# Optimization experiments

Measured on AMD Instinct MI355X. Metric: run time of the kernel, lower is better.

## Reference

```python
import jax, jax.numpy as jnp
import numpy as np

EPS = 1e-5  # torch BatchNorm1d default eps
NH, KD, D_V = 8, 64, 128  # num_heads, key_dim, per-head value dim (attn_ratio*key_dim)


def hardswish(x):
    return x * jnp.clip(x + 3.0, 0.0, 6.0) / 6.0


def linear_bn(x, W, g, b):
    # Linear (no bias) followed by BatchNorm1d in training mode: batch stats
    # over all leading dims (torch flattens (B,N) before BN).
    y = x @ W.T
    yf = y.reshape(-1, y.shape[-1])
    mu = yf.mean(0)
    var = yf.var(0)  # biased variance, matching BN normalization
    return (y - mu) * (g / jnp.sqrt(var + EPS)) + b


def setup_inputs() -> dict:
    key = jax.random.key(0)
    ks = jax.random.split(key, 22)
    B, C, H, W, NT, D = 8, 1024, 96, 96, 60, 512
    dh = NH * D_V          # 1024
    h_kv = dh + NH * KD    # 1536
    hf = 2 * D             # 1024 (mr=2)

    def p(k, shape, s=0.02):
        return jax.random.normal(k, shape, jnp.float32) * s

    return {
        "im_emd": jax.random.normal(ks[0], (B, C, H, W), jnp.float32),
        "text_emd": jax.random.normal(ks[1], (NT, D), jnp.float32),
        "W_dc": p(ks[2], (D, C)), "g_dc": 1.0 + p(ks[3], (D,)), "b_dc": p(ks[4], (D,)),
        "W_kv": p(ks[5], (h_kv, D)), "g_kv": 1.0 + p(ks[6], (h_kv,)), "b_kv": p(ks[7], (h_kv,)),
        "W_q": p(ks[8], (NH * KD, D)), "g_q": 1.0 + p(ks[9], (NH * KD,)), "b_q": p(ks[10], (NH * KD,)),
        "W_proj": p(ks[11], (D, dh)), "g_proj": 1.0 + p(ks[12], (D,)), "b_proj": p(ks[13], (D,)),
        "biases": p(ks[14], (NH, 10000)),  # relative-position bias table (100x100 offsets)
        "W_f1": p(ks[15], (hf, D)), "g_f1": 1.0 + p(ks[16], (hf,)), "b_f1": p(ks[17], (hf,)),
        "W_f2": p(ks[18], (D, hf)), "g_f2": 1.0 + p(ks[19], (D,)), "b_f2": p(ks[20], (D,)),
    }


def _bias_idx(NT, H, W):
    # Offset table built row-major over product(range(100), range(100)) =>
    # attention_offsets[(a,b)] == 100*a + b. Text token t maps to grid point
    # (t//100, t%100); image token n to (n//W, n%W).
    t = np.arange(NT)
    n = np.arange(H * W)
    dx = np.abs(t[:, None] // 100 - n[None, :] // W)
    dy = np.abs(t[:, None] % 100 - n[None, :] % W)
    return 100 * dx + dy  # [NT, N]


def reference(im_emd, text_emd, W_dc, g_dc, b_dc, W_kv, g_kv, b_kv,
              W_q, g_q, b_q, W_proj, g_proj, b_proj, biases,
              W_f1, g_f1, b_f1, W_f2, g_f2, b_f2):
    B, C, H, W = im_emd.shape
    N = H * W
    NT, D = text_emd.shape
    dh = NH * D_V
    scale = KD ** -0.5

    # image tokens -> embed_dim
    x = im_emd.reshape(B, C, N).transpose(0, 2, 1)          # [B,N,C]
    xd = hardswish(linear_bn(x, W_dc, g_dc, b_dc))          # [B,N,D]

    # Attentioninv: text queries attend over image keys/values
    kv = linear_bn(xd, W_kv, g_kv, b_kv).reshape(B, N, NH, KD + D_V)
    k, v = kv[..., :KD], kv[..., KD:]                       # [B,N,h,64], [B,N,h,128]
    q = linear_bn(text_emd[None], W_q, g_q, b_q).reshape(NT, NH, KD)  # [NT,h,64]

    idx = jnp.asarray(_bias_idx(NT, H, W))                  # [NT,N] static
    bias = biases[:, idx]                                   # [h,NT,N] gather

    attn = jnp.einsum('thd,bnhd->bhtn', q, k) * scale + bias[None]
    attn = jax.nn.softmax(attn, axis=-1)                    # [B,h,NT,N]
    out = jnp.einsum('bhtn,bnhd->bthd', attn, v).reshape(B, NT, dh)
    out = linear_bn(hardswish(out), W_proj, g_proj, b_proj)  # [B,NT,D]

    textd = text_emd[None] + out                            # residual (broadcast)

    # ffntext: Linear_BN -> Hardswish -> Linear_BN(bn_weight_init=0) + residual
    f = hardswish(linear_bn(textd, W_f1, g_f1, b_f1))
    f = linear_bn(f, W_f2, g_f2, b_f2)
    textd = f + textd
    return textd[0]  # [NT, D]
```

## Files before the change

### kernel.cpp

```cpp
#include <hip/hip_runtime.h>
#include <hip/hip_bf16.h>
#include <stdint.h>

typedef short bf16x8 __attribute__((ext_vector_type(8)));
typedef float f32x4 __attribute__((ext_vector_type(4)));

__device__ __forceinline__ float b2f(ushort u){ return __uint_as_float(((uint32_t)u)<<16); }
__device__ __forceinline__ ushort f2b(float f){
  uint32_t u = __float_as_uint(f);
  u += 0x7fffu + ((u>>16)&1u);
  return (ushort)(u>>16);
}
__device__ __forceinline__ float hswish(float x){ return x*fminf(fmaxf(x+3.f,0.f),6.f)*(1.f/6.f); }

__device__ __forceinline__ void gll16(const void* g, void* l){
  __builtin_amdgcn_global_load_lds((const __attribute__((address_space(1))) void*)g,
                                   (__attribute__((address_space(3))) void*)l, 16, 0, 0);
}

__global__ void init_kernel(const float* __restrict__ Wdc, const float* __restrict__ Wkv,
                            ushort* __restrict__ Wdc_b, ushort* __restrict__ Wkv_b,
                            float* __restrict__ zbase){
  int i = blockIdx.x*256 + threadIdx.x;
  if (i < 8192) zbase[i] = 0.f;
  for (int j=i; j<512*1024; j+=262144) Wdc_b[j] = f2b(Wdc[j]);
  for (int j=i; j<1536*512; j+=262144) Wkv_b[j] = f2b(Wkv[j]);
}

__global__ __launch_bounds__(256) void transpose_kernel(const float* __restrict__ im, ushort* __restrict__ At){
  __shared__ float tb[64][65];
  const int b = blockIdx.z, c0 = blockIdx.y*64, n0 = blockIdx.x*64;
  const int tid = threadIdx.x;
  const int cl = tid >> 2, q = tid & 3;
  #pragma unroll
  for (int it=0; it<4; ++it){
    int nn = q*4 + it*16;
    float4 v = *(const float4*)&im[((size_t)(b*1024 + c0 + cl))*9216 + n0 + nn];
    tb[cl][nn+0]=v.x; tb[cl][nn+1]=v.y; tb[cl][nn+2]=v.z; tb[cl][nn+3]=v.w;
  }
  __syncthreads();
  const int nr = tid >> 4, c4 = (tid & 15)*4;
  #pragma unroll
  for (int ps=0; ps<4; ++ps){
    int nn = nr + ps*16;
    ushort4 u;
    u.x = f2b(tb[c4+0][nn]); u.y = f2b(tb[c4+1][nn]);
    u.z = f2b(tb[c4+2][nn]); u.w = f2b(tb[c4+3][nn]);
    *(ushort4*)&At[((size_t)(b*9216 + n0 + nn))*1024 + c0 + c4] = u;
  }
}

template<int SPLIT>
__global__ __launch_bounds__(512) void gemm_bt(
    const ushort* __restrict__ A, const ushort* __restrict__ Bm,
    ushort* __restrict__ Cm, ushort* __restrict__ Vt,
    float* __restrict__ sums, float* __restrict__ sqs,
    int NT, int N, int K)
{
  extern __shared__ __align__(16) ushort smem[];
  ushort* As = smem;
  ushort* Bs = smem + 3*16384;
  const int tid = threadIdx.x;
  const int l = tid & 63;
  const int w = tid >> 6;
  const int wm = w >> 1, wn = w & 1;
  const int chunk = gridDim.x >> 3;
  const int wg = (blockIdx.x & 7)*chunk + (blockIdx.x >> 3);
  const int tn = wg % NT, tm = wg / NT;
  const size_t n0 = (size_t)tn * 128;
  const size_t m0 = (size_t)tm * 256;
  const int lr = l & 15, lk = l >> 4;
  const int wb = tid & ~63;

  f32x4 acc[4][4];
  #pragma unroll
  for (int i=0;i<4;++i)
    #pragma unroll
    for (int j=0;j<4;++j) acc[i][j] = (f32x4){0.f,0.f,0.f,0.f};

  const int nt = K >> 6;

  auto STAGE = [&](int s, int kt_idx){
    const int kt = kt_idx << 6;
    #pragma unroll
    for (int it=0; it<4; ++it){
      int idx = it*512 + tid;
      int row = idx >> 3, c8 = idx & 7;
      int sc8 = c8 ^ (row & 7);
      gll16(&A[(m0+row)*K + kt + sc8*8], &As[s*16384 + (it*512 + wb)*8]);
    }
    #pragma unroll
    for (int it=0; it<2; ++it){
      int idx = it*512 + tid;
      int row = idx >> 3, c8 = idx & 7;
      int sc8 = c8 ^ (row & 7);
      gll16(&Bm[(n0+row)*K + kt + sc8*8], &Bs[s*8192 + (it*512 + wb)*8]);
    }
  };

  STAGE(0, 0);
  if (nt > 1) STAGE(1, 1);

  for (int t = 0; t < nt; ++t){
    if (t+2 < nt) STAGE((t+2)%3, t+2);
    const int newer = (t+2 < nt) ? 2 : ((t+1 < nt) ? 1 : 0);
    if (newer == 2)      asm volatile("s_waitcnt vmcnt(12)" ::: "memory");
    else if (newer == 1) asm volatile("s_waitcnt vmcnt(6)"  ::: "memory");
    else                 asm volatile("s_waitcnt vmcnt(0)"  ::: "memory");
    __builtin_amdgcn_s_barrier();
    asm volatile("" ::: "memory");
    const ushort* as = As + (t%3)*16384;
    const ushort* bs = Bs + (t%3)*8192;
    __builtin_amdgcn_s_setprio(1);
    #pragma unroll
    for (int kk=0; kk<64; kk+=32){
      bf16x8 af[4], bfr[4];
      #pragma unroll
      for (int i=0;i<4;++i){
        int row = wm*64 + i*16 + lr;
        af[i] = *(const bf16x8*)&as[row*64 + ((kk + lk*8) ^ ((row&7)<<3))];
      }
      #pragma unroll
      for (int j=0;j<4;++j){
        int row = wn*64 + j*16 + lr;
        bfr[j] = *(const bf16x8*)&bs[row*64 + ((kk + lk*8) ^ ((row&7)<<3))];
      }
      #pragma unroll
      for (int i=0;i<4;++i)
        #pragma unroll
        for (int j=0;j<4;++j)
          acc[i][j] = __builtin_amdgcn_mfma_f32_16x16x32_bf16(af[i], bfr[j], acc[i][j], 0, 0, 0);
    }
    __builtin_amdgcn_s_setprio(0);
    asm volatile("s_waitcnt lgkmcnt(0)" ::: "memory");
    __builtin_amdgcn_s_barrier();
    asm volatile("" ::: "memory");
  }

  if constexpr (SPLIT==0){
    #pragma unroll
    for (int i=0;i<4;++i)
      #pragma unroll
      for (int j=0;j<4;++j)
        #pragma unroll
        for (int r=0;r<4;++r) {
          size_t row = m0 + wm*64 + i*16 + lk*4 + r;
          size_t col = n0 + wn*64 + j*16 + lr;
          Cm[row*N + col] = f2b(acc[i][j][r]);
        }
  } else {
    const int bq = (int)(m0/9216);
    const int nbase = (int)(m0 - (size_t)bq*9216);
    #pragma unroll
    for (int j=0;j<4;++j){
      int c = (int)n0 + wn*64 + j*16 + lr;
      int h = c/192, rcol = c - h*192;
      #pragma unroll
      for (int i=0;i<4;++i){
        int nrow = nbase + wm*64 + i*16 + lk*4;
        if (rcol < 64){
          ushort* kb = Cm + ((size_t)(bq*9216 + nrow))*512 + h*64 + rcol;
          #pragma unroll
          for (int r=0;r<4;++r) kb[(size_t)r*512] = f2b(acc[i][j][r]);
        } else {
          int dv = rcol - 64;
          ushort4 u;
          u.x=f2b(acc[i][j][0]); u.y=f2b(acc[i][j][1]);
          u.z=f2b(acc[i][j][2]); u.w=f2b(acc[i][j][3]);
          *(ushort4*)&Vt[((size_t)((bq*8+h)*128 + dv))*9216 + nrow] = u;
        }
      }
    }
  }
  #pragma unroll
  for (int j=0;j<4;++j){
    float cs=0.f, cq=0.f;
    #pragma unroll
    for (int i=0;i<4;++i)
      #pragma unroll
      for (int r=0;r<4;++r){ float v=acc[i][j][r]; cs+=v; cq+=v*v; }
    cs += __shfl_xor(cs,16); cs += __shfl_xor(cs,32);
    cq += __shfl_xor(cq,16); cq += __shfl_xor(cq,32);
    if (lk==0){
      int col = (int)n0 + wn*64 + j*16 + lr;
      atomicAdd(&sums[col], cs);
      atomicAdd(&sqs [col], cq);
    }
  }
}

__global__ void bn_finalize(const float* __restrict__ sums, const float* __restrict__ sqs,
                            const float* __restrict__ g, const float* __restrict__ bb,
                            float* __restrict__ scale, float* __restrict__ shift, int C, float invn)
{
  int c = blockIdx.x*256 + threadIdx.x;
  if (c < C){
    float mu = sums[c]*invn;
    float var = sqs[c]*invn - mu*mu;
    float k = g[c] * rsqrtf(var + 1e-5f);
    scale[c] = k;
    shift[c] = bb[c] - mu*k;
  }
}

__global__ __launch_bounds__(256) void bn_hswish(ushort* __restrict__ y, const float* __restrict__ scale, const float* __restrict__ shift)
{
  __shared__ float sc[512], sh[512];
  for (int i=threadIdx.x;i<512;i+=256){ sc[i]=scale[i]; sh[i]=shift[i]; }
  __syncthreads();
  const size_t total = (size_t)73728*512/8;
  for (size_t idx = (size_t)blockIdx.x*256+threadIdx.x; idx < total; idx += (size_t)gridDim.x*256){
    uint4 u = *(uint4*)&y[idx*8];
    ushort* up = (ushort*)&u;
    int c0 = ((int)(idx & 63))*8;
    #pragma unroll
    for (int e=0;e<8;++e){
      float x = b2f(up[e])*sc[c0+e] + sh[c0+e];
      up[e] = f2b(hswish(x));
    }
    *(uint4*)&y[idx*8] = u;
  }
}

__global__ __launch_bounds__(256) void q_gemm(const float* __restrict__ text, const float* __restrict__ Wq, float* __restrict__ qraw)
{
  __shared__ __align__(16) float xr[512];
  const int t = blockIdx.x, tid = threadIdx.x;
  for (int i=tid;i<512;i+=256) xr[i] = text[t*512+i];
  __syncthreads();
  #pragma unroll
  for (int cj=0;cj<2;++cj){
    int c = cj*256+tid;
    const float4* wp = (const float4*)(Wq + (size_t)c*512);
    const float4* xp = (const float4*)xr;
    float a=0.f;
    for (int u=0;u<128;++u){
      float4 wv = wp[u], xv = xp[u];
      a += wv.x*xv.x + wv.y*xv.y + wv.z*xv.z + wv.w*xv.w;
    }
    qraw[t*512+c]=a;
  }
}

__global__ __launch_bounds__(512) void q_bn_qh(const float* __restrict__ qraw, const float* __restrict__ g,
                                               const float* __restrict__ bb,
                                               const float* __restrict__ scale2, const float* __restrict__ shift2,
                                               ushort* __restrict__ Qh, float* __restrict__ cQ)
{
  const int c = threadIdx.x;
  const int h = c >> 6, d = c & 63;
  float s=0.f,q=0.f;
  for (int t=0;t<60;++t){ float v = qraw[t*512+c]; s+=v; q+=v*v; }
  float mu=s*(1.f/60.f), var=q*(1.f/60.f)-mu*mu;
  float k = g[c]*rsqrtf(var+1e-5f);
  float sh = bb[c]-mu*k;
  const float sk = scale2[h*192+d]*0.125f;
  const float tk = shift2[h*192+d]*0.125f;
  for (int t=0;t<60;++t){
    float qv = qraw[t*512+c]*k+sh;
    Qh[(h*64+t)*64+d] = f2b(qv*sk);
    float contrib = qv*tk;
    #pragma unroll
    for (int o=32;o>0;o>>=1) contrib += __shfl_xor(contrib,o);
    if (d==0) cQ[h*64+t] = contrib;
  }
  for (int t=60;t<64;++t) Qh[(h*64+t)*64+d] = 0;
  if (d==0) for (int t=60;t<64;++t) cQ[h*64+t] = 0.f;
}

__global__ __launch_bounds__(256) void attn_flash(
    const ushort* __restrict__ Qh, const float* __restrict__ cQ,
    const ushort* __restrict__ Kbuf, const ushort* __restrict__ Vt,
    const float* __restrict__ biases,
    float* __restrict__ Op, float* __restrict__ Mp, float* __restrict__ Lp)
{
  __shared__ __align__(16) ushort Qs[64*72];
  __shared__ __align__(16) ushort vt[128*64];
  __shared__ __align__(16) ushort Pw[4][16*72];
  __shared__ float bias_l[1200];
  __shared__ float cQs[64];
  const int tid = threadIdx.x;
  const int l = tid & 63, w = tid >> 6;
  const int lr = l & 15, lk = l >> 4;
  const int nc = blockIdx.x, h = blockIdx.y, b = blockIdx.z;
  const int bh = b*8+h;
  const int wbase = tid & ~63;
  for (int cid = tid; cid < 512; cid += 256){
    int row = cid >> 3, c8 = cid & 7;
    *(uint4*)&Qs[row*72 + c8*8] = *(const uint4*)&Qh[(size_t)(h*64+row)*64 + c8*8];
  }
  for (int i = tid; i < 1200; i += 256) bias_l[i] = biases[h*10000 + nc*1200 + i];
  if (tid < 64) cQs[tid] = cQ[h*64 + tid];

  const ushort* vsrc = Vt + (size_t)bh*128*9216;
  const ushort* kchunk = Kbuf + (size_t)b*9216*512 + h*64;

  float m_run[4] = {-1e30f,-1e30f,-1e30f,-1e30f};
  float l_run[4] = {0.f,0.f,0.f,0.f};
  f32x4 acc_o[8];
  #pragma unroll
  for (int j=0;j<8;++j) acc_o[j] = (f32x4){0.f,0.f,0.f,0.f};
  __syncthreads();

  for (int tile=0; tile<18; ++tile){
    const int n0 = nc*1152 + tile*64;
    if (tile) __syncthreads();
    #pragma unroll
    for (int it=0; it<4; ++it){
      int idx = it*256 + tid;
      int row = idx >> 3, c8 = idx & 7;
      int sc8 = c8 ^ (row & 7);
      gll16(&vsrc[(size_t)row*9216 + n0 + sc8*8], &vt[(it*256 + wbase)*8]);
    }
    __syncthreads();
    f32x4 sa[4];
    #pragma unroll
    for (int j=0;j<4;++j) sa[j]=(f32x4){0.f,0.f,0.f,0.f};
    const ushort* kbase = kchunk + (size_t)n0*512;
    __builtin_amdgcn_s_setprio(1);
    #pragma unroll
    for (int kk=0; kk<64; kk+=32){
      bf16x8 af = *(const bf16x8*)&Qs[(w*16+lr)*72 + kk + lk*8];
      #pragma unroll
      for (int j=0;j<4;++j){
        bf16x8 bf_ = *(const bf16x8*)&kbase[(size_t)(j*16+lr)*512 + kk + lk*8];
        sa[j] = __builtin_amdgcn_mfma_f32_16x16x32_bf16(af, bf_, sa[j], 0,0,0);
      }
    }
    __builtin_amdgcn_s_setprio(0);
    float mt[4] = {-1e30f,-1e30f,-1e30f,-1e30f};
    #pragma unroll
    for (int j=0;j<4;++j){
      int n = n0 + j*16 + lr;
      int py = n/96;
      int px = n - py*96;
      int pyl = py - nc*12;
      #pragma unroll
      for (int r=0;r<4;++r){
        int t = w*16 + lk*4 + r;
        int dd = t - px; dd = dd<0?-dd:dd;
        float s = sa[j][r] + cQs[t] + bias_l[pyl*100 + dd];
        sa[j][r] = s;
        mt[r] = fmaxf(mt[r], s);
      }
    }
    #pragma unroll
    for (int r=0;r<4;++r){
      #pragma unroll
      for (int o=1;o<16;o<<=1) mt[r] = fmaxf(mt[r], __shfl_xor(mt[r], o));
      float mnew = fmaxf(m_run[r], mt[r]);
      float ef = __expf(m_run[r] - mnew);
      m_run[r] = mnew;
      l_run[r] *= ef;
      #pragma unroll
      for (int j2=0;j2<8;++j2) acc_o[j2][r] *= ef;
    }
    float rs[4] = {0.f,0.f,0.f,0.f};
    #pragma unroll
    for (int j=0;j<4;++j)
      #pragma unroll
      for (int r=0;r<4;++r){
        float pe = __expf(sa[j][r] - m_run[r]);
        rs[r] += pe;
        Pw[w][(lk*4+r)*72 + j*16 + lr] = f2b(pe);
      }
    #pragma unroll
    for (int r=0;r<4;++r){
      #pragma unroll
      for (int o=1;o<16;o<<=1) rs[r] += __shfl_xor(rs[r], o);
      l_run[r] += rs[r];
    }
    __builtin_amdgcn_s_setprio(1);
    #pragma unroll
    for (int kk=0; kk<64; kk+=32){
      bf16x8 pa = *(const bf16x8*)&Pw[w][lr*72 + kk + lk*8];
      #pragma unroll
      for (int j2=0;j2<8;++j2){
        int dv = j2*16 + lr;
        bf16x8 vb = *(const bf16x8*)&vt[dv*64 + ((kk + lk*8) ^ ((dv&7)<<3))];
        acc_o[j2] = __builtin_amdgcn_mfma_f32_16x16x32_bf16(pa, vb, acc_o[j2], 0,0,0);
      }
    }
    __builtin_amdgcn_s_setprio(0);
  }
  float* ob = Op + (((size_t)nc*64 + bh)*64)*128;
  #pragma unroll
  for (int j2=0;j2<8;++j2)
    #pragma unroll
    for (int r=0;r<4;++r){
      int row = w*16 + lk*4 + r;
      ob[(size_t)row*128 + j2*16 + lr] = acc_o[j2][r];
    }
  if (lr == 0){
    #pragma unroll
    for (int r=0;r<4;++r){
      int row = w*16 + lk*4 + r;
      Mp[(nc*64+bh)*64 + row] = m_run[r];
      Lp[(nc*64+bh)*64 + row] = l_run[r];
    }
  }
}

__global__ __launch_bounds__(128) void attn_combine(
    const float* __restrict__ Op, const float* __restrict__ Mp, const float* __restrict__ Lp,
    float* __restrict__ attn_o)
{
  const int t = blockIdx.x, bh = blockIdx.y;
  const int b = bh >> 3, h = bh & 7;
  const int dv = threadIdx.x;
  float mv[8];
  float m_g = -1e30f;
  #pragma unroll
  for (int i=0;i<8;++i){ mv[i] = Mp[(i*64+bh)*64 + t]; m_g = fmaxf(m_g, mv[i]); }
  float lsum = 0.f;
  #pragma unroll
  for (int i=0;i<8;++i) lsum += Lp[(i*64+bh)*64 + t] * __expf(mv[i]-m_g);
  float o = 0.f;
  #pragma unroll
  for (int i=0;i<8;++i)
    o += Op[(((size_t)i*64 + bh)*64 + t)*128 + dv] * __expf(mv[i]-m_g);
  attn_o[(size_t)(b*60+t)*1024 + h*128 + dv] = o / lsum;
}

template<int CIN, int COUT, int MODE>
__global__ __launch_bounds__(256) void rowgemm8(
    const float* __restrict__ X, const float* __restrict__ Wt,
    const float* __restrict__ sc, const float* __restrict__ sh,
    const float* __restrict__ text, float* __restrict__ textd,
    float* __restrict__ out, float* __restrict__ osum, float* __restrict__ osq)
{
  __shared__ __align__(16) float xr[8][CIN];
  const int rb0 = blockIdx.x*8, tid = threadIdx.x;
  for (int i=tid; i<8*CIN; i+=256){
    int rr = i / CIN, cc = i % CIN;
    float v = X[(size_t)(rb0+rr)*CIN + cc];
    if constexpr (MODE==2){ v = v*sc[cc]+sh[cc]; v = hswish(v); }
    if constexpr (MODE==3){ int idx = 64 + (cc&127) + (cc>>7)*192; v = v*sc[idx]+sh[idx]; v = hswish(v); }
    if constexpr (MODE==4){
      int t = (rb0+rr) % 60;
      v = text[t*CIN+cc] + v*sc[cc]+sh[cc];
      if (blockIdx.y == 0) textd[(size_t)(rb0+rr)*CIN + cc] = v;
    }
    xr[rr][cc]=v;
  }
  __syncthreads();
  int c = blockIdx.y*256 + tid;
  const float4* wp = (const float4*)(Wt + (size_t)c*CIN);
  float a[8] = {0.f,0.f,0.f,0.f,0.f,0.f,0.f,0.f};
  for (int u=0;u<CIN/4;++u){
    float4 wv = wp[u];
    #pragma unroll
    for (int rr=0;rr<8;++rr){
      float4 xv = *(const float4*)&xr[rr][u*4];
      a[rr] += wv.x*xv.x + wv.y*xv.y + wv.z*xv.z + wv.w*xv.w;
    }
  }
  float ps=0.f, pq=0.f;
  #pragma unroll
  for (int rr=0;rr<8;++rr){
    out[(size_t)(rb0+rr)*COUT + c] = a[rr];
    ps += a[rr]; pq += a[rr]*a[rr];
  }
  atomicAdd(&osum[c], ps);
  atomicAdd(&osq [c], pq);
}

__global__ void final_out(const float* __restrict__ f2raw, const float* __restrict__ sf, const float* __restrict__ tf,
                          const float* __restrict__ textd, float* __restrict__ outp)
{
  int i = blockIdx.x*256+threadIdx.x;
  if (i < 60*512){ int c = i & 511; outp[i] = f2raw[i]*sf[c]+tf[c] + textd[i]; }
}

extern "C" void kernel_launch(void* const* d_in, const int* in_sizes, int n_in,
                              void* d_out, int out_size, void* d_ws, size_t ws_size,
                              hipStream_t stream)
{
  (void)in_sizes; (void)n_in; (void)out_size; (void)ws_size;
  const float* im    = (const float*)d_in[0];
  const float* text  = (const float*)d_in[1];
  const float* W_dc  = (const float*)d_in[2];
  const float* g_dc  = (const float*)d_in[3];
  const float* b_dc  = (const float*)d_in[4];
  const float* W_kv  = (const float*)d_in[5];
  const float* g_kv  = (const float*)d_in[6];
  const float* b_kv  = (const float*)d_in[7];
  const float* W_q   = (const float*)d_in[8];
  const float* g_q   = (const float*)d_in[9];
  const float* b_q   = (const float*)d_in[10];
  const float* W_proj= (const float*)d_in[11];
  const float* g_proj= (const float*)d_in[12];
  const float* b_proj= (const float*)d_in[13];
  const float* biases= (const float*)d_in[14];
  const float* W_f1  = (const float*)d_in[15];
  const float* g_f1  = (const float*)d_in[16];
  const float* b_f1  = (const float*)d_in[17];
  const float* W_f2  = (const float*)d_in[18];
  const float* g_f2  = (const float*)d_in[19];
  const float* b_f2  = (const float*)d_in[20];
  float* outp = (float*)d_out;

  char* p = (char*)d_ws;
  auto alloc = [&](size_t bytes)->char*{ char* r = p; p += (bytes+255)&~(size_t)255; return r; };
  float* s1_sum = (float*)alloc(512*4);
  float* s1_sq  = (float*)alloc(512*4);
  float* s2_sum = (float*)alloc(1536*4);
  float* s2_sq  = (float*)alloc(1536*4);
  float* s3_sum = (float*)alloc(512*4);
  float* s3_sq  = (float*)alloc(512*4);
  float* s4_sum = (float*)alloc(1024*4);
  float* s4_sq  = (float*)alloc(1024*4);
  float* s5_sum = (float*)alloc(512*4);
  float* s5_sq  = (float*)alloc(512*4);
  float* zero_base = s1_sum;
  float* attn_o = (float*)alloc((size_t)480*1024*4);
  float* sc1 = (float*)alloc(512*4);
  float* sh1 = (float*)alloc(512*4);
  float* sc2 = (float*)alloc(1536*4);
  float* sh2 = (float*)alloc(1536*4);
  float* qraw = (float*)alloc(60*512*4);
  ushort* Qh = (ushort*)alloc((size_t)8*64*64*2);
  float* cQ = (float*)alloc(512*4);
  float* proj_raw = (float*)alloc((size_t)480*512*4);
  float* sp=(float*)alloc(512*4); float* tp=(float*)alloc(512*4);
  float* textd=(float*)alloc((size_t)480*512*4);
  float* sf1=(float*)alloc(1024*4); float* tf1=(float*)alloc(1024*4);
  float* f1_raw=(float*)alloc((size_t)480*1024*4);
  float* sf2=(float*)alloc(512*4); float* tf2=(float*)alloc(512*4);
  float* f2_raw=(float*)alloc((size_t)480*512*4);
  float* Op = (float*)alloc((size_t)8*64*64*128*4);
  float* Mp = (float*)alloc((size_t)8*64*64*4);
  float* Lp = (float*)alloc((size_t)8*64*64*4);
  ushort* Wdc_b = (ushort*)alloc((size_t)512*1024*2);
  ushort* Wkv_b = (ushort*)alloc((size_t)1536*512*2);
  ushort* y1 = (ushort*)alloc((size_t)73728*512*2);
  ushort* Kbuf = (ushort*)alloc((size_t)73728*512*2);
  ushort* Vt  = (ushort*)alloc((size_t)64*128*9216*2);
  ushort* At = (ushort*)alloc((size_t)73728*1024*2);

  const size_t GEMM_LDS = 3*(16384+8192)*sizeof(ushort);

  init_kernel<<<1024,256,0,stream>>>(W_dc, W_kv, Wdc_b, Wkv_b, zero_base);
  transpose_kernel<<<dim3(144,16,8),256,0,stream>>>(im, At);
  gemm_bt<0><<<1152,512,GEMM_LDS,stream>>>(At, Wdc_b, y1, nullptr, s1_sum, s1_sq, 4, 512, 1024);
  bn_finalize<<<2,256,0,stream>>>(s1_sum, s1_sq, g_dc, b_dc, sc1, sh1, 512, 1.f/73728.f);
  bn_hswish<<<2048,256,0,stream>>>(y1, sc1, sh1);
  gemm_bt<1><<<3456,512,GEMM_LDS,stream>>>(y1, Wkv_b, Kbuf, Vt, s2_sum, s2_sq, 12, 1536, 512);
  bn_finalize<<<6,256,0,stream>>>(s2_sum, s2_sq, g_kv, b_kv, sc2, sh2, 1536, 1.f/73728.f);
  q_gemm<<<60,256,0,stream>>>(text, W_q, qraw);
  q_bn_qh<<<1,512,0,stream>>>(qraw, g_q, b_q, sc2, sh2, Qh, cQ);
  attn_flash<<<dim3(8,8,8),256,0,stream>>>(Qh, cQ, Kbuf, Vt, biases, Op, Mp, Lp);
  attn_combine<<<dim3(60,64),128,0,stream>>>(Op, Mp, Lp, attn_o);
  rowgemm8<1024,512,3><<<dim3(60,2),256,0,stream>>>(attn_o, W_proj, sc2, sh2, nullptr, nullptr, proj_raw, s3_sum, s3_sq);
  bn_finalize<<<2,256,0,stream>>>(s3_sum, s3_sq, g_proj, b_proj, sp, tp, 512, 1.f/480.f);
  rowgemm8<512,1024,4><<<dim3(60,4),256,0,stream>>>(proj_raw, W_f1, sp, tp, text, textd, f1_raw, s4_sum, s4_sq);
  bn_finalize<<<4,256,0,stream>>>(s4_sum, s4_sq, g_f1, b_f1, sf1, tf1, 1024, 1.f/480.f);
  rowgemm8<1024,512,2><<<dim3(60,2),256,0,stream>>>(f1_raw, W_f2, sf1, tf1, nullptr, nullptr, f2_raw, s5_sum, s5_sq);
  bn_finalize<<<2,256,0,stream>>>(s5_sum, s5_sq, g_f2, b_f2, sf2, tf2, 512, 1.f/480.f);
  final_out<<<120,256,0,stream>>>(f2_raw, sf2, tf2, textd, outp);
}
```

Measured before the change: 791.2 us.

## Enlarge GEMM tile to 256x256 with interleaved double-buffered loads

The bf16 GEMM tile grows from 256x128 to 256x256, with each wave computing 128x64 outputs (32 accumulators). The triple-buffered LDS pipeline becomes a double buffer whose next-tile global loads are split into four phases, each interleaved with a block of MFMAs. Larger tiles raise arithmetic intensity and halve the number of workgroups for both big GEMMs, cutting global and LDS traffic per FLOP. In exchange it raises register pressure and occupancy may drop, and the extra barriers per k-step add synchronisation cost.

New measurement: 754.9 us. -4.6%, faster.

```diff
diff --git a/kernel.cpp b/kernel.cpp
--- a/kernel.cpp
+++ b/kernel.cpp
@@ -59,130 +59,155 @@
 {
   extern __shared__ __align__(16) ushort smem[];
   ushort* As = smem;
-  ushort* Bs = smem + 3*16384;
+  ushort* Bs = smem + 32768;
   const int tid = threadIdx.x;
   const int l = tid & 63;
   const int w = tid >> 6;
-  const int wm = w >> 1, wn = w & 1;
+  const int wm = w >> 2, wn = w & 3;
   const int chunk = gridDim.x >> 3;
   const int wg = (blockIdx.x & 7)*chunk + (blockIdx.x >> 3);
   const int tn = wg % NT, tm = wg / NT;
-  const size_t n0 = (size_t)tn * 128;
+  const size_t n0 = (size_t)tn * 256;
   const size_t m0 = (size_t)tm * 256;
   const int lr = l & 15, lk = l >> 4;
   const int wb = tid & ~63;
-
-  f32x4 acc[4][4];
-  #pragma unroll
-  for (int i=0;i<4;++i)
+  const int swz = (lr & 7) << 3;
+
+  f32x4 acc[8][4];
+  #pragma unroll
+  for (int i=0;i<8;++i)
     #pragma unroll
     for (int j=0;j<4;++j) acc[i][j] = (f32x4){0.f,0.f,0.f,0.f};
 
   const int nt = K >> 6;
 
-  auto STAGE = [&](int s, int kt_idx){
-    const int kt = kt_idx << 6;
-    #pragma unroll
-    for (int it=0; it<4; ++it){
-      int idx = it*512 + tid;
-      int row = idx >> 3, c8 = idx & 7;
-      int sc8 = c8 ^ (row & 7);
-      gll16(&A[(m0+row)*K + kt + sc8*8], &As[s*16384 + (it*512 + wb)*8]);
-    }
-    #pragma unroll
-    for (int it=0; it<2; ++it){
-      int idx = it*512 + tid;
-      int row = idx >> 3, c8 = idx & 7;
-      int sc8 = c8 ^ (row & 7);
-      gll16(&Bm[(n0+row)*K + kt + sc8*8], &Bs[s*8192 + (it*512 + wb)*8]);
-    }
+  auto STAGE = [&](int bsel, int kti, int p){
+    const int kt = kti << 6;
+    int idx = p*512 + tid;
+    int row = idx >> 3, c8 = idx & 7;
+    int sc8 = c8 ^ (row & 7);
+    gll16(&A[(m0+row)*K + kt + sc8*8], &As[bsel*16384 + (p*512 + wb)*8]);
+    gll16(&Bm[(n0+row)*K + kt + sc8*8], &Bs[bsel*16384 + (p*512 + wb)*8]);
   };
 
-  STAGE(0, 0);
-  if (nt > 1) STAGE(1, 1);
+  #pragma unroll
+  for (int p=0;p<4;++p) STAGE(0, 0, p);
 
   for (int t = 0; t < nt; ++t){
-    if (t+2 < nt) STAGE((t+2)%3, t+2);
-    const int newer = (t+2 < nt) ? 2 : ((t+1 < nt) ? 1 : 0);
-    if (newer == 2)      asm volatile("s_waitcnt vmcnt(12)" ::: "memory");
-    else if (newer == 1) asm volatile("s_waitcnt vmcnt(6)"  ::: "memory");
-    else                 asm volatile("s_waitcnt vmcnt(0)"  ::: "memory");
+    const int cur = t & 1;
+    const ushort* as = As + cur*16384;
+    const ushort* bs = Bs + cur*16384;
+    const bool pre = (t+1 < nt);
+    if (pre){
+      STAGE(cur^1, t+1, 0);
+      asm volatile("s_waitcnt vmcnt(2)" ::: "memory");
+    } else {
+      asm volatile("s_waitcnt vmcnt(0)" ::: "memory");
+    }
     __builtin_amdgcn_s_barrier();
     asm volatile("" ::: "memory");
-    const ushort* as = As + (t%3)*16384;
-    const ushort* bs = Bs + (t%3)*8192;
-    __builtin_amdgcn_s_setprio(1);
-    #pragma unroll
-    for (int kk=0; kk<64; kk+=32){
-      bf16x8 af[4], bfr[4];
-      #pragma unroll
-      for (int i=0;i<4;++i){
-        int row = wm*64 + i*16 + lr;
-        af[i] = *(const bf16x8*)&as[row*64 + ((kk + lk*8) ^ ((row&7)<<3))];
+    bf16x8 bfr[4][2];
+    #pragma unroll
+    for (int cf=0; cf<4; ++cf)
+      #pragma unroll
+      for (int x=0; x<2; ++x){
+        int row = wn*64 + cf*16 + lr;
+        bfr[cf][x] = *(const bf16x8*)&bs[row*64 + ((x*32 + lk*8) ^ swz)];
       }
-      #pragma unroll
-      for (int j=0;j<4;++j){
-        int row = wn*64 + j*16 + lr;
-        bfr[j] = *(const bf16x8*)&bs[row*64 + ((kk + lk*8) ^ ((row&7)<<3))];
-      }
-      #pragma unroll
-      for (int i=0;i<4;++i)
+    {
+      bf16x8 af[2][2];
+      #pragma unroll
+      for (int i=0;i<2;++i)
         #pragma unroll
-        for (int j=0;j<4;++j)
-          acc[i][j] = __builtin_amdgcn_mfma_f32_16x16x32_bf16(af[i], bfr[j], acc[i][j], 0, 0, 0);
-    }
-    __builtin_amdgcn_s_setprio(0);
-    asm volatile("s_waitcnt lgkmcnt(0)" ::: "memory");
+        for (int x=0;x<2;++x){
+          int row = wm*128 + i*16 + lr;
+          af[i][x] = *(const bf16x8*)&as[row*64 + ((x*32 + lk*8) ^ swz)];
+        }
+      __builtin_amdgcn_s_setprio(1);
+      #pragma unroll
+      for (int x=0;x<2;++x)
+        #pragma unroll
+        for (int i=0;i<2;++i)
+          #pragma unroll
+          for (int cf=0;cf<4;++cf)
+            acc[i][cf] = __builtin_amdgcn_mfma_f32_16x16x32_bf16(af[i][x], bfr[cf][x], acc[i][cf], 0,0,0);
+      __builtin_amdgcn_s_setprio(0);
+    }
     __builtin_amdgcn_s_barrier();
     asm volatile("" ::: "memory");
+    #pragma unroll
+    for (int p=1; p<4; ++p){
+      if (pre) STAGE(cur^1, t+1, p);
+      bf16x8 af[2][2];
+      #pragma unroll
+      for (int i=0;i<2;++i)
+        #pragma unroll
+        for (int x=0;x<2;++x){
+          int row = wm*128 + (2*p+i)*16 + lr;
+          af[i][x] = *(const bf16x8*)&as[row*64 + ((x*32 + lk*8) ^ swz)];
+        }
+      __builtin_amdgcn_s_barrier();
+      asm volatile("" ::: "memory");
+      __builtin_amdgcn_s_setprio(1);
+      #pragma unroll
+      for (int x=0;x<2;++x)
+        #pragma unroll
+        for (int i=0;i<2;++i)
+          #pragma unroll
+          for (int cf=0;cf<4;++cf)
+            acc[2*p+i][cf] = __builtin_amdgcn_mfma_f32_16x16x32_bf16(af[i][x], bfr[cf][x], acc[2*p+i][cf], 0,0,0);
+      __builtin_amdgcn_s_setprio(0);
+      __builtin_amdgcn_s_barrier();
+      asm volatile("" ::: "memory");
+    }
   }
 
   if constexpr (SPLIT==0){
     #pragma unroll
-    for (int i=0;i<4;++i)
-      #pragma unroll
-      for (int j=0;j<4;++j)
+    for (int rf=0;rf<8;++rf)
+      #pragma unroll
+      for (int cf=0;cf<4;++cf)
         #pragma unroll
         for (int r=0;r<4;++r) {
-          size_t row = m0 + wm*64 + i*16 + lk*4 + r;
-          size_t col = n0 + wn*64 + j*16 + lr;
-          Cm[row*N + col] = f2b(acc[i][j][r]);
+          size_t row = m0 + wm*128 + rf*16 + lk*4 + r;
+          size_t col = n0 + wn*64 + cf*16 + lr;
+          Cm[row*N + col] = f2b(acc[rf][cf][r]);
         }
   } else {
     const int bq = (int)(m0/9216);
     const int nbase = (int)(m0 - (size_t)bq*9216);
     #pragma unroll
-    for (int j=0;j<4;++j){
-      int c = (int)n0 + wn*64 + j*16 + lr;
+    for (int cf=0;cf<4;++cf){
+      int c = (int)n0 + wn*64 + cf*16 + lr;
       int h = c/192, rcol = c - h*192;
       #pragma unroll
-      for (int i=0;i<4;++i){
-        int nrow = nbase + wm*64 + i*16 + lk*4;
+      for (int rf=0;rf<8;++rf){
+        int nrow = nbase + wm*128 + rf*16 + lk*4;
         if (rcol < 64){
           ushort* kb = Cm + ((size_t)(bq*9216 + nrow))*512 + h*64 + rcol;
           #pragma unroll
-          for (int r=0;r<4;++r) kb[(size_t)r*512] = f2b(acc[i][j][r]);
+          for (int r=0;r<4;++r) kb[(size_t)r*512] = f2b(acc[rf][cf][r]);
         } else {
           int dv = rcol - 64;
           ushort4 u;
-          u.x=f2b(acc[i][j][0]); u.y=f2b(acc[i][j][1]);
-          u.z=f2b(acc[i][j][2]); u.w=f2b(acc[i][j][3]);
+          u.x=f2b(acc[rf][cf][0]); u.y=f2b(acc[rf][cf][1]);
+          u.z=f2b(acc[rf][cf][2]); u.w=f2b(acc[rf][cf][3]);
           *(ushort4*)&Vt[((size_t)((bq*8+h)*128 + dv))*9216 + nrow] = u;
         }
       }
     }
   }
   #pragma unroll
-  for (int j=0;j<4;++j){
+  for (int cf=0;cf<4;++cf){
     float cs=0.f, cq=0.f;
     #pragma unroll
-    for (int i=0;i<4;++i)
-      #pragma unroll
-      for (int r=0;r<4;++r){ float v=acc[i][j][r]; cs+=v; cq+=v*v; }
+    for (int rf=0;rf<8;++rf)
+      #pragma unroll
+      for (int r=0;r<4;++r){ float v=acc[rf][cf][r]; cs+=v; cq+=v*v; }
     cs += __shfl_xor(cs,16); cs += __shfl_xor(cs,32);
     cq += __shfl_xor(cq,16); cq += __shfl_xor(cq,32);
     if (lk==0){
-      int col = (int)n0 + wn*64 + j*16 + lr;
+      int col = (int)n0 + wn*64 + cf*16 + lr;
       atomicAdd(&sums[col], cs);
       atomicAdd(&sqs [col], cq);
     }
@@ -538,14 +563,14 @@
   ushort* Vt  = (ushort*)alloc((size_t)64*128*9216*2);
   ushort* At = (ushort*)alloc((size_t)73728*1024*2);
 
-  const size_t GEMM_LDS = 3*(16384+8192)*sizeof(ushort);
+  const size_t GEMM_LDS = 2*(16384+16384)*sizeof(ushort);
 
   init_kernel<<<1024,256,0,stream>>>(W_dc, W_kv, Wdc_b, Wkv_b, zero_base);
   transpose_kernel<<<dim3(144,16,8),256,0,stream>>>(im, At);
-  gemm_bt<0><<<1152,512,GEMM_LDS,stream>>>(At, Wdc_b, y1, nullptr, s1_sum, s1_sq, 4, 512, 1024);
+  gemm_bt<0><<<576,512,GEMM_LDS,stream>>>(At, Wdc_b, y1, nullptr, s1_sum, s1_sq, 2, 512, 1024);
   bn_finalize<<<2,256,0,stream>>>(s1_sum, s1_sq, g_dc, b_dc, sc1, sh1, 512, 1.f/73728.f);
   bn_hswish<<<2048,256,0,stream>>>(y1, sc1, sh1);
-  gemm_bt<1><<<3456,512,GEMM_LDS,stream>>>(y1, Wkv_b, Kbuf, Vt, s2_sum, s2_sq, 12, 1536, 512);
+  gemm_bt<1><<<1728,512,GEMM_LDS,stream>>>(y1, Wkv_b, Kbuf, Vt, s2_sum, s2_sq, 6, 1536, 512);
   bn_finalize<<<6,256,0,stream>>>(s2_sum, s2_sq, g_kv, b_kv, sc2, sh2, 1536, 1.f/73728.f);
   q_gemm<<<60,256,0,stream>>>(text, W_q, qraw);
   q_bn_qh<<<1,512,0,stream>>>(qraw, g_q, b_q, sc2, sh2, Qh, cQ);
```
